# Optimization experiments

Measured on AMD Instinct MI355X. Metric: run time of the kernel, lower is better.

## Reference

```python
import jax, jax.numpy as jnp
import numpy as np
from jax import lax

C = 64          # grid_channels
RGB = 3         # rgb_channels
D = 128         # conditioning_dim
NUM_CLASSES = 1000
HIDDEN = 256    # hypernet hidden
NUM_STEPS = 32
TOT1 = C * C * 9


def setup_inputs() -> dict:
    key = jax.random.key(0)
    ks = jax.random.split(key, 20)
    s = 0.02
    B, H, W = 32, 64, 64
    return {
        "class_labels": jax.random.randint(ks[0], (B,), 0, NUM_CLASSES),
        "initial_grid": jax.random.normal(ks[1], (B, C, H, W), jnp.float32) * 0.1,
        "emb": jax.random.normal(ks[2], (NUM_CLASSES, D), jnp.float32) * s,
        "hw1": jax.random.normal(ks[3], (D, HIDDEN), jnp.float32) * s,
        "hb1": jnp.zeros((HIDDEN,), jnp.float32),
        "hw2": jax.random.normal(ks[4], (HIDDEN, HIDDEN), jnp.float32) * s,
        "hb2": jnp.zeros((HIDDEN,), jnp.float32),
        "hw3": jax.random.normal(ks[5], (HIDDEN, 2 * TOT1), jnp.float32) * s,
        "hb3": jnp.zeros((2 * TOT1,), jnp.float32),
        "f1w1": jax.random.normal(ks[6], (D, D), jnp.float32) * s,
        "f1b1": jnp.zeros((D,), jnp.float32),
        "f1w2": jax.random.normal(ks[7], (D, 2 * C), jnp.float32) * s,
        "f1b2": jnp.concatenate([jnp.ones((C,), jnp.float32), jnp.zeros((C,), jnp.float32)]),
        "f2w1": jax.random.normal(ks[8], (D, D), jnp.float32) * s,
        "f2b1": jnp.zeros((D,), jnp.float32),
        "f2w2": jax.random.normal(ks[9], (D, 2 * C), jnp.float32) * s,
        "f2b2": jnp.concatenate([jnp.ones((C,), jnp.float32), jnp.zeros((C,), jnp.float32)]),
        "blend": jnp.float32(0.5),
    }


def _conv_circ_one(x, w):
    # x: [C,H,W], w: [Cout,Cin,3,3]; circular pad then VALID conv == padding=1 circular
    xp = jnp.pad(x, ((0, 0), (1, 1), (1, 1)), mode='wrap')
    return lax.conv_general_dilated(xp[None], w, (1, 1), 'VALID')[0]

_bconv = jax.vmap(_conv_circ_one)  # per-sample dynamic weights over batch


def _film_params(cond, w1, b1, w2, b2):
    p = jax.nn.relu(cond @ w1 + b1) @ w2 + b2  # [B, 2C]
    return p[:, :C, None, None], p[:, C:, None, None]


def reference(class_labels, initial_grid, emb, hw1, hb1, hw2, hb2, hw3, hb3,
              f1w1, f1b1, f1w2, f1b2, f2w1, f2b1, f2w2, f2b2, blend):
    cond = emb[class_labels]                       # [B, D]
    h = jax.nn.relu(cond @ hw1 + hb1)
    h = jax.nn.relu(h @ hw2 + hb2)
    weights = h @ hw3 + hb3                        # [B, 2*C*C*9]
    B = cond.shape[0]
    w1 = weights[:, :TOT1].reshape(B, C, C, 3, 3)
    w2 = weights[:, TOT1:].reshape(B, C, C, 3, 3)
    g1, be1 = _film_params(cond, f1w1, f1b1, f1w2, f1b2)
    g2, be2 = _film_params(cond, f2w1, f2b1, f2w2, f2b2)
    blend_s = jax.nn.sigmoid(blend)

    def step(grid, _):
        u = jax.nn.relu(g1 * _bconv(grid, w1) + be1)
        u = jax.nn.relu(g2 * _bconv(u, w2) + be2)
        grid = (1 - blend_s) * grid + blend_s * u
        rgb = jax.nn.sigmoid(grid[:, :RGB])
        return grid, rgb

    _, traj = lax.scan(step, initial_grid, None, length=NUM_STEPS)  # [T,B,3,H,W]
    return traj[-1], traj
```

## Files before the change

kernel.cpp:

```cpp
#include <hip/hip_runtime.h>


typedef __attribute__((ext_vector_type(8))) short short8;
typedef __attribute__((ext_vector_type(4))) float f32x4;
typedef __attribute__((ext_vector_type(8))) unsigned short us8;

__device__ __forceinline__ unsigned short f2bf(float f) {
  unsigned int u = __builtin_bit_cast(unsigned int, f);
  u = (u + 0x7FFFu + ((u >> 16) & 1u)) >> 16;
  return (unsigned short)u;
}
__device__ __forceinline__ float bf2f(unsigned short h) {
  unsigned int u = ((unsigned int)h) << 16;
  return __builtin_bit_cast(float, u);
}

__device__ __forceinline__ void gl_lds16(const void* g, void* l) {
  __builtin_amdgcn_global_load_lds((const __attribute__((address_space(1))) void*)g,
                                   (__attribute__((address_space(3))) void*)l, 16, 0, 0);
}

__global__ void hyper_kernel(const int* __restrict__ labels, const float* __restrict__ emb,
                             const float* __restrict__ hw1, const float* __restrict__ hb1,
                             const float* __restrict__ hw2, const float* __restrict__ hb2,
                             float* __restrict__ h2T) {
  __shared__ float cond[128];
  __shared__ float h1[256];
  const int s = blockIdx.x, j = threadIdx.x;
  if (j < 128) cond[j] = emb[(size_t)labels[s] * 128 + j];
  __syncthreads();
  float a = hb1[j];
  for (int k = 0; k < 128; ++k) a += cond[k] * hw1[k * 256 + j];
  h1[j] = fmaxf(a, 0.f);
  __syncthreads();
  float a2 = hb2[j];
  for (int k = 0; k < 256; ++k) a2 += h1[k] * hw2[k * 256 + j];
  h2T[j * 32 + s] = fmaxf(a2, 0.f);
}

__global__ void film_kernel(const int* __restrict__ labels, const float* __restrict__ emb,
                            const float* __restrict__ f1w1, const float* __restrict__ f1b1,
                            const float* __restrict__ f1w2, const float* __restrict__ f1b2,
                            const float* __restrict__ f2w1, const float* __restrict__ f2b1,
                            const float* __restrict__ f2w2, const float* __restrict__ f2b2,
                            float* __restrict__ film) {
  __shared__ float cond[128];
  __shared__ float hid[128];
  const int s = blockIdx.x, which = blockIdx.y, j = threadIdx.x;
  const float* W1 = which ? f2w1 : f1w1;
  const float* B1 = which ? f2b1 : f1b1;
  const float* W2 = which ? f2w2 : f1w2;
  const float* B2 = which ? f2b2 : f1b2;
  cond[j] = emb[(size_t)labels[s] * 128 + j];
  __syncthreads();
  float a = B1[j];
  for (int k = 0; k < 128; ++k) a += cond[k] * W1[k * 128 + j];
  hid[j] = fmaxf(a, 0.f);
  __syncthreads();
  float p = B2[j];
  for (int k = 0; k < 128; ++k) p += hid[k] * W2[k * 128 + j];
  film[(size_t)((which * 2 + (j >> 6)) * 32 + s) * 64 + (j & 63)] = p;
}

__launch_bounds__(256)
__global__ void wgen_kernel(const float* __restrict__ h2T, const float* __restrict__ hw3,
                            const float* __restrict__ hb3, unsigned short* __restrict__ W) {
  __shared__ float h2l[8192];
  __shared__ float wbuf[2][32 * 128];
  const int t = threadIdx.x;
  for (int i = t; i < 8192; i += 256) h2l[i] = h2T[i];
  const int lane = t & 63, wid = t >> 6;
  const int col = t & 127;
  const int sg  = t >> 7;
  const int j   = blockIdx.x * 128 + col;
  const float* __restrict__ hp = h2l + sg * 16;

  const int i0   = (lane >> 5);
  const int csub = (lane & 31) << 2;
#define WG_STAGE(BUF, KC)                                                      \
  _Pragma("unroll")                                                            \
  for (int q = 0; q < 4; ++q) {                                                \
    const int ii = q * 4 + wid;                                                \
    gl_lds16(hw3 + (size_t)((KC) + 2 * ii + i0) * 73728 + blockIdx.x * 128 + csub, \
             &wbuf[BUF][2 * ii * 128]);                                        \
  }

  float acc[16];
  #pragma unroll
  for (int i = 0; i < 16; ++i) acc[i] = 0.f;

  WG_STAGE(0, 0)
  asm volatile("s_waitcnt vmcnt(0)" ::: "memory");
  __syncthreads();

  int buf = 0;
  #pragma unroll 1
  for (int kc = 0; kc < 256; kc += 32) {
    if (kc + 32 < 256) WG_STAGE(buf ^ 1, kc + 32)
    #pragma unroll
    for (int kk = 0; kk < 32; ++kk) {
      const float wv = wbuf[buf][kk * 128 + col];
      const float4 hA = *(const float4*)(hp + (kc + kk) * 32);
      const float4 hB = *(const float4*)(hp + (kc + kk) * 32 + 4);
      const float4 hC = *(const float4*)(hp + (kc + kk) * 32 + 8);
      const float4 hD = *(const float4*)(hp + (kc + kk) * 32 + 12);
      acc[0]  += hA.x * wv; acc[1]  += hA.y * wv; acc[2]  += hA.z * wv; acc[3]  += hA.w * wv;
      acc[4]  += hB.x * wv; acc[5]  += hB.y * wv; acc[6]  += hB.z * wv; acc[7]  += hB.w * wv;
      acc[8]  += hC.x * wv; acc[9]  += hC.y * wv; acc[10] += hC.z * wv; acc[11] += hC.w * wv;
      acc[12] += hD.x * wv; acc[13] += hD.y * wv; acc[14] += hD.z * wv; acc[15] += hD.w * wv;
    }
    asm volatile("s_waitcnt vmcnt(0)" ::: "memory");
    __syncthreads();
    buf ^= 1;
  }
#undef WG_STAGE

  const float bias = hb3[j];
  const int cv = j / 36864;
  const int r  = j - cv * 36864;
  const int co = r / 576;
  const int r2 = r - co * 576;
  const int ci = r2 / 9;
  const int tap = r2 - ci * 9;
  const int sw = (co * 64 + ci) ^ ((co & 7) << 3);
  #pragma unroll
  for (int i = 0; i < 16; ++i) {
    const int s2 = sg * 16 + i;
    W[(size_t)((s2 * 2 + cv) * 9 + tap) * 4096 + sw] = f2bf(acc[i] + bias);
  }
}

__global__ void init_kernel(const float* __restrict__ gin, unsigned short* __restrict__ g0) {
  __shared__ float lds[64][65];
  const int b = blockIdx.x >> 6, y = blockIdx.x & 63;
  const int t = threadIdx.x;
  {
    const int ci = t >> 2, xq = t & 3;
    const float* base = gin + (size_t)((b * 64 + ci) * 64 + y) * 64;
    #pragma unroll
    for (int q = 0; q < 4; ++q) {
      const int x0 = (xq + q * 4) * 4;
      const float4 v = *(const float4*)(base + x0);
      lds[ci][x0+0] = v.x; lds[ci][x0+1] = v.y; lds[ci][x0+2] = v.z; lds[ci][x0+3] = v.w;
    }
  }
  __syncthreads();
  const int x = t >> 2, cq = t & 3, ci0 = cq * 16;
  us8 lo, hi;
  #pragma unroll
  for (int i = 0; i < 8; ++i) lo[i] = f2bf(lds[ci0 + i][x]);
  #pragma unroll
  for (int i = 0; i < 8; ++i) hi[i] = f2bf(lds[ci0 + 8 + i][x]);
  char* dbase = (char*)(g0 + (size_t)(b * 64 + y) * 4096);
  const int o = x * 128 + ci0 * 2, sw = (x & 7) << 4;
  *(us8*)(dbase + (o ^ sw)) = lo;
  *(us8*)(dbase + ((o + 16) ^ sw)) = hi;
}

template<int WHICH>
__launch_bounds__(512, 2)
__global__ void conv_kernel(const unsigned short* __restrict__ Wall,
                            const unsigned short* __restrict__ src,
                            unsigned short* __restrict__ dst,
                            const unsigned short* __restrict__ gold,
                            const float* __restrict__ film,
                            const float* __restrict__ blendp,
                            float* __restrict__ out, int t) {
  __shared__ unsigned short in_lds[10 * 4096];
  __shared__ unsigned short w_lds[9 * 4096];
  const int tid  = threadIdx.x;
  const int wid  = tid >> 6;
  const int lane = tid & 63;
  const int l15  = lane & 15;
  const int lhi  = lane >> 4;
  const int b    = blockIdx.x;
  const int s    = (b & 7) + 8 * ((b >> 3) & 3);
  const int y0   = (b >> 5) * 8;

  const unsigned short* srcs = src + (size_t)s * 262144;
  const unsigned short* Wb   = Wall + (size_t)((s * 2 + WHICH) * 9) * 4096;

  #pragma unroll
  for (int q = 0; q < 10; ++q) {
    const int c   = q * 8 + wid;
    const int row = c >> 3, part = c & 7;
    const int gy  = (y0 + row + 63) & 63;
    gl_lds16(srcs + gy * 4096 + part * 512 + lane * 8, &in_lds[row * 4096 + part * 512]);
  }
  #pragma unroll
  for (int q = 0; q < 9; ++q) {
    const int c = q * 8 + wid;
    gl_lds16(Wb + c * 512 + lane * 8, &w_lds[c * 512]);
  }
  asm volatile("s_waitcnt vmcnt(0)" ::: "memory");
  __syncthreads();

  f32x4 acc[4][4];
  #pragma unroll
  for (int m = 0; m < 4; ++m)
    #pragma unroll
    for (int n = 0; n < 4; ++n)
      #pragma unroll
      for (int j = 0; j < 4; ++j) acc[m][n][j] = 0.f;

  short8 afA[4][2], bfA[4][2], afB[4][2], bfB[4][2];

#define CONV_LOAD(AF, BF, TAP)                                                  \
  {                                                                             \
    const int ky = (TAP) / 3, kx = (TAP) % 3;                                   \
    _Pragma("unroll")                                                           \
    for (int m = 0; m < 4; ++m) {                                               \
      const int co = m * 16 + l15;                                              \
      _Pragma("unroll")                                                         \
      for (int kk = 0; kk < 2; ++kk) {                                          \
        const int off = (TAP) * 8192 +                                          \
            ((co * 128 + kk * 64 + lhi * 16) ^ ((co & 7) << 4));                \
        AF[m][kk] = *(const short8*)((const char*)w_lds + off);                 \
      }                                                                         \
    }                                                                           \
    const int r = wid + ky;                                                     \
    _Pragma("unroll")                                                           \
    for (int n = 0; n < 4; ++n) {                                               \
      const int xs = (n * 16 + l15 + kx + 63) & 63;                             \
      _Pragma("unroll")                                                         \
      for (int kk = 0; kk < 2; ++kk) {                                          \
        const int off = r * 8192 +                                              \
            ((xs * 128 + kk * 64 + lhi * 16) ^ ((xs & 7) << 4));                \
        BF[n][kk] = *(const short8*)((const char*)in_lds + off);                \
      }                                                                         \
    }                                                                           \
  }

#define CONV_MMAC(AF, BF)                                                       \
  __builtin_amdgcn_s_setprio(1);                                                \
  _Pragma("unroll")                                                             \
  for (int kk = 0; kk < 2; ++kk)                                                \
    _Pragma("unroll")                                                           \
    for (int m = 0; m < 4; ++m)                                                 \
      _Pragma("unroll")                                                         \
      for (int n = 0; n < 4; ++n)                                               \
        acc[m][n] = __builtin_amdgcn_mfma_f32_16x16x32_bf16(                    \
            AF[m][kk], BF[n][kk], acc[m][n], 0, 0, 0);                          \
  __builtin_amdgcn_s_setprio(0);

  CONV_LOAD(afA, bfA, 0)
  CONV_LOAD(afB, bfB, 1)  CONV_MMAC(afA, bfA)
  CONV_LOAD(afA, bfA, 2)  CONV_MMAC(afB, bfB)
  CONV_LOAD(afB, bfB, 3)  CONV_MMAC(afA, bfA)
  CONV_LOAD(afA, bfA, 4)  CONV_MMAC(afB, bfB)
  CONV_LOAD(afB, bfB, 5)  CONV_MMAC(afA, bfA)
  CONV_LOAD(afA, bfA, 6)  CONV_MMAC(afB, bfB)
  CONV_LOAD(afB, bfB, 7)  CONV_MMAC(afA, bfA)
  CONV_LOAD(afA, bfA, 8)  CONV_MMAC(afB, bfB)
  CONV_MMAC(afA, bfA)
#undef CONV_LOAD
#undef CONV_MMAC

  const int y = y0 + wid;
  const float* fg = film + WHICH * 2 * 2048;
  const float* fb = fg + 2048;
  float bs = 0.f, obs = 0.f;
  if (WHICH == 1) { bs = 1.f / (1.f + expf(-blendp[0])); obs = 1.f - bs; }
  unsigned short* drow = dst + (size_t)s * 262144 + y * 4096;
  const unsigned short* grow = (WHICH == 1) ? (gold + (size_t)s * 262144 + y * 4096) : (const unsigned short*)nullptr;

  #pragma unroll
  for (int m = 0; m < 4; ++m) {
    const int co0 = m * 16 + lhi * 4;
    const float4 g  = *(const float4*)&fg[s * 64 + co0];
    const float4 be = *(const float4*)&fb[s * 64 + co0];
    #pragma unroll
    for (int n = 0; n < 4; ++n) {
      const int x = n * 16 + l15;
      const int off = (x * 128 + co0 * 2) ^ ((x & 7) << 4);
      const f32x4 v = acc[m][n];
      const float u0 = fmaxf(g.x * v[0] + be.x, 0.f);
      const float u1 = fmaxf(g.y * v[1] + be.y, 0.f);
      const float u2 = fmaxf(g.z * v[2] + be.z, 0.f);
      const float u3 = fmaxf(g.w * v[3] + be.w, 0.f);
      if (WHICH == 0) {
        ushort4 pk; pk.x = f2bf(u0); pk.y = f2bf(u1); pk.z = f2bf(u2); pk.w = f2bf(u3);
        *(ushort4*)((char*)drow + off) = pk;
      } else {
        const ushort4 od = *(const ushort4*)((const char*)grow + off);
        const float g0 = obs * bf2f(od.x) + bs * u0;
        const float g1 = obs * bf2f(od.y) + bs * u1;
        const float g2 = obs * bf2f(od.z) + bs * u2;
        const float g3 = obs * bf2f(od.w) + bs * u3;
        ushort4 pk; pk.x = f2bf(g0); pk.y = f2bf(g1); pk.z = f2bf(g2); pk.w = f2bf(g3);
        *(ushort4*)((char*)drow + off) = pk;
        if (co0 == 0) {
          const float r0 = 1.f / (1.f + expf(-g0));
          const float r1 = 1.f / (1.f + expf(-g1));
          const float r2 = 1.f / (1.f + expf(-g2));
          float* ob = out + 393216 + (size_t)((t * 32 + s) * 3) * 4096 + y * 64 + x;
          ob[0] = r0; ob[4096] = r1; ob[8192] = r2;
          if (t == 31) {
            float* o2 = out + (size_t)(s * 3) * 4096 + y * 64 + x;
            o2[0] = r0; o2[4096] = r1; o2[8192] = r2;
          }
        }
      }
    }
  }
}

extern "C" void kernel_launch(void* const* d_in, const int* in_sizes, int n_in,
                              void* d_out, int out_size, void* d_ws, size_t ws_size,
                              hipStream_t stream) {
  (void)in_sizes; (void)n_in; (void)out_size; (void)ws_size;
  const int*   labels = (const int*)d_in[0];
  const float* gin    = (const float*)d_in[1];
  const float* emb    = (const float*)d_in[2];
  const float* hw1    = (const float*)d_in[3];
  const float* hb1    = (const float*)d_in[4];
  const float* hw2    = (const float*)d_in[5];
  const float* hb2    = (const float*)d_in[6];
  const float* hw3    = (const float*)d_in[7];
  const float* hb3    = (const float*)d_in[8];
  const float* f1w1   = (const float*)d_in[9];
  const float* f1b1   = (const float*)d_in[10];
  const float* f1w2   = (const float*)d_in[11];
  const float* f1b2   = (const float*)d_in[12];
  const float* f2w1   = (const float*)d_in[13];
  const float* f2b1   = (const float*)d_in[14];
  const float* f2w2   = (const float*)d_in[15];
  const float* f2b2   = (const float*)d_in[16];
  const float* blend  = (const float*)d_in[17];
  float* out = (float*)d_out;

  char* ws = (char*)d_ws;
  unsigned short* grid0 = (unsigned short*)(ws + (size_t)0);
  unsigned short* grid1 = (unsigned short*)(ws + (size_t)16777216);
  unsigned short* ubuf  = (unsigned short*)(ws + (size_t)33554432);
  unsigned short* Wbuf  = (unsigned short*)(ws + (size_t)50331648);
  float* h2T  = (float*)(ws + (size_t)55050240);
  float* film = (float*)(ws + (size_t)55083008);

  hyper_kernel<<<32, 256, 0, stream>>>(labels, emb, hw1, hb1, hw2, hb2, h2T);
  film_kernel<<<dim3(32, 2), 128, 0, stream>>>(labels, emb, f1w1, f1b1, f1w2, f1b2,
                                               f2w1, f2b1, f2w2, f2b2, film);
  wgen_kernel<<<576, 256, 0, stream>>>(h2T, hw3, hb3, Wbuf);
  init_kernel<<<2048, 256, 0, stream>>>(gin, grid0);

  for (int t = 0; t < 32; ++t) {
    unsigned short* gi = (t & 1) ? grid1 : grid0;
    unsigned short* go = (t & 1) ? grid0 : grid1;
    conv_kernel<0><<<256, 512, 0, stream>>>(Wbuf, gi, ubuf, nullptr, film, nullptr, nullptr, t);
    conv_kernel<1><<<256, 512, 0, stream>>>(Wbuf, ubuf, go, gi, film, blend, out, t);
  }
}
```

Measured before the change: 1.217 ms.

## Use bf16 MFMA for hypernet weight-generation GEMM with register prefetch

Result: no change. 1.204 ms (-1.0%).

```diff
diff --git a/kernel.cpp b/kernel.cpp
--- a/kernel.cpp
+++ b/kernel.cpp
@@ -65,68 +65,70 @@
 __launch_bounds__(256)
 __global__ void wgen_kernel(const float* __restrict__ h2T, const float* __restrict__ hw3,
                             const float* __restrict__ hb3, unsigned short* __restrict__ W) {
-  __shared__ float h2l[8192];
-  __shared__ float wbuf[2][32 * 128];
+  __shared__ unsigned int h2f[4096];
   const int t = threadIdx.x;
-  for (int i = t; i < 8192; i += 256) h2l[i] = h2T[i];
+  #pragma unroll
+  for (int d = 0; d < 16; ++d) {
+    const int idx = d * 256 + t;
+    const int jd = idx & 3, ln = (idx >> 2) & 63, kh = idx >> 8;
+    const int k  = (kh >> 1) * 32 + (ln >> 4) * 8 + jd * 2;
+    const int s  = (kh & 1) * 16 + (ln & 15);
+    const float f0 = h2T[k * 32 + s];
+    const float f1 = h2T[(k + 1) * 32 + s];
+    h2f[idx] = (unsigned int)f2bf(f0) | ((unsigned int)f2bf(f1) << 16);
+  }
+  __syncthreads();
+
   const int lane = t & 63, wid = t >> 6;
-  const int col = t & 127;
-  const int sg  = t >> 7;
-  const int j   = blockIdx.x * 128 + col;
-  const float* __restrict__ hp = h2l + sg * 16;
-
-  const int i0   = (lane >> 5);
-  const int csub = (lane & 31) << 2;
-#define WG_STAGE(BUF, KC)                                                      \
-  _Pragma("unroll")                                                            \
-  for (int q = 0; q < 4; ++q) {                                                \
-    const int ii = q * 4 + wid;                                                \
-    gl_lds16(hw3 + (size_t)((KC) + 2 * ii + i0) * 73728 + blockIdx.x * 128 + csub, \
-             &wbuf[BUF][2 * ii * 128]);                                        \
-  }
-
-  float acc[16];
-  #pragma unroll
-  for (int i = 0; i < 16; ++i) acc[i] = 0.f;
-
-  WG_STAGE(0, 0)
-  asm volatile("s_waitcnt vmcnt(0)" ::: "memory");
-  __syncthreads();
-
-  int buf = 0;
-  #pragma unroll 1
-  for (int kc = 0; kc < 256; kc += 32) {
-    if (kc + 32 < 256) WG_STAGE(buf ^ 1, kc + 32)
-    #pragma unroll
-    for (int kk = 0; kk < 32; ++kk) {
-      const float wv = wbuf[buf][kk * 128 + col];
-      const float4 hA = *(const float4*)(hp + (kc + kk) * 32);
-      const float4 hB = *(const float4*)(hp + (kc + kk) * 32 + 4);
-      const float4 hC = *(const float4*)(hp + (kc + kk) * 32 + 8);
-      const float4 hD = *(const float4*)(hp + (kc + kk) * 32 + 12);
-      acc[0]  += hA.x * wv; acc[1]  += hA.y * wv; acc[2]  += hA.z * wv; acc[3]  += hA.w * wv;
-      acc[4]  += hB.x * wv; acc[5]  += hB.y * wv; acc[6]  += hB.z * wv; acc[7]  += hB.w * wv;
-      acc[8]  += hC.x * wv; acc[9]  += hC.y * wv; acc[10] += hC.z * wv; acc[11] += hC.w * wv;
-      acc[12] += hD.x * wv; acc[13] += hD.y * wv; acc[14] += hD.z * wv; acc[15] += hD.w * wv;
-    }
-    asm volatile("s_waitcnt vmcnt(0)" ::: "memory");
-    __syncthreads();
-    buf ^= 1;
-  }
-#undef WG_STAGE
-
-  const float bias = hb3[j];
-  const int cv = j / 36864;
-  const int r  = j - cv * 36864;
-  const int co = r / 576;
-  const int r2 = r - co * 576;
-  const int ci = r2 / 9;
-  const int tap = r2 - ci * 9;
-  const int sw = (co * 64 + ci) ^ ((co & 7) << 3);
-  #pragma unroll
-  for (int i = 0; i < 16; ++i) {
-    const int s2 = sg * 16 + i;
-    W[(size_t)((s2 * 2 + cv) * 9 + tap) * 4096 + sw] = f2bf(acc[i] + bias);
+  const int l15 = lane & 15, lhi = lane >> 4;
+  const int col0 = blockIdx.x * 64 + wid * 16;
+  const float* __restrict__ ap = hw3 + (size_t)(lhi * 8) * 73728 + col0 + l15;
+
+  f32x4 acc0 = {0.f, 0.f, 0.f, 0.f}, acc1 = {0.f, 0.f, 0.f, 0.f};
+  float aA[8], aB[8];
+  #pragma unroll
+  for (int j2 = 0; j2 < 8; ++j2) aA[j2] = ap[(size_t)j2 * 73728];
+
+#define WG_STEP(CUR, NXT, KS)                                                  \
+  {                                                                            \
+    if ((KS) < 7) {                                                            \
+      _Pragma("unroll")                                                        \
+      for (int j2 = 0; j2 < 8; ++j2)                                           \
+        NXT[j2] = ap[(size_t)(((KS) + 1) * 32 + j2) * 73728];                  \
+    }                                                                          \
+    us8 av;                                                                    \
+    _Pragma("unroll")                                                          \
+    for (int j2 = 0; j2 < 8; ++j2) av[j2] = f2bf(CUR[j2]);                     \
+    const short8 afr = __builtin_bit_cast(short8, av);                         \
+    const short8 b0 = *(const short8*)&h2f[((KS) * 2 + 0) * 256 + lane * 4];   \
+    const short8 b1 = *(const short8*)&h2f[((KS) * 2 + 1) * 256 + lane * 4];   \
+    acc0 = __builtin_amdgcn_mfma_f32_16x16x32_bf16(afr, b0, acc0, 0, 0, 0);    \
+    acc1 = __builtin_amdgcn_mfma_f32_16x16x32_bf16(afr, b1, acc1, 0, 0, 0);    \
+  }
+
+  WG_STEP(aA, aB, 0)
+  WG_STEP(aB, aA, 1)
+  WG_STEP(aA, aB, 2)
+  WG_STEP(aB, aA, 3)
+  WG_STEP(aA, aB, 4)
+  WG_STEP(aB, aA, 5)
+  WG_STEP(aA, aB, 6)
+  WG_STEP(aB, aA, 7)
+#undef WG_STEP
+
+  #pragma unroll
+  for (int r = 0; r < 4; ++r) {
+    const int j = col0 + lhi * 4 + r;
+    const float bias = hb3[j];
+    const int cv  = j / 36864;
+    const int rr  = j - cv * 36864;
+    const int co  = rr / 576;
+    const int r2  = rr - co * 576;
+    const int ci  = r2 / 9;
+    const int tap = r2 - ci * 9;
+    const int sw  = (co * 64 + ci) ^ ((co & 7) << 3);
+    W[(size_t)(((l15)      * 2 + cv) * 9 + tap) * 4096 + sw] = f2bf(acc0[r] + bias);
+    W[(size_t)(((l15 + 16) * 2 + cv) * 9 + tap) * 4096 + sw] = f2bf(acc1[r] + bias);
   }
 }
 
@@ -340,7 +342,7 @@
   hyper_kernel<<<32, 256, 0, stream>>>(labels, emb, hw1, hb1, hw2, hb2, h2T);
   film_kernel<<<dim3(32, 2), 128, 0, stream>>>(labels, emb, f1w1, f1b1, f1w2, f1b2,
                                                f2w1, f2b1, f2w2, f2b2, film);
-  wgen_kernel<<<576, 256, 0, stream>>>(h2T, hw3, hb3, Wbuf);
+  wgen_kernel<<<1152, 256, 0, stream>>>(h2T, hw3, hb3, Wbuf);
   init_kernel<<<2048, 256, 0, stream>>>(gin, grid0);
 
   for (int t = 0; t < 32; ++t) {
```
